# Optimization experiments

Measured on AMD Instinct MI355X. Metric: run time of the kernel, lower is better.

## Reference

```python
import jax, jax.numpy as jnp
import numpy as np

N, T, F_IN = 20000, 13, 3
E = 320000
NB, NL = 4, 2
C_RES, C_DIL, C_SKIP, C_END = 32, 32, 256, 512
KSZ, KHOP = 2, 4
N_PRED, N_OUT = 12, 2
L = NB * NL
DILS = [2 ** i for _ in range(NB) for i in range(NL)]  # [1,2,1,2,1,2,1,2]
EPS = 1e-5


def _dconv(x, w, d):
    # x: [N,C,T], w: [O,I,K]; valid dilated conv -> [N,O,T-(K-1)*d]
    return jax.lax.conv_general_dilated(x, w, (1,), 'VALID', rhs_dilation=(d,),
                                        dimension_numbers=('NCH', 'OIH', 'NCH'))


def _forward(inputs, edge_src, edge_dst, enter_w, enter_b, filt_w, filt_b, gate_w, gate_b,
             gc_w, gc_b, skip_w, skip_b, bn_g, bn_b, out1_w, out1_b, out2_w, out2_b):
    # inputs: [N,T,F] -> x: [N,C_RES,T] via 1x1 conv (enter)
    x = jnp.einsum('of,ntf->not', enter_w, inputs) + enter_b[None, :, None]
    deg = jax.ops.segment_sum(jnp.ones((E,), x.dtype), edge_dst, num_segments=N)
    deg = jnp.maximum(deg, 1.0)[:, None, None]

    def propagate(h):  # [N,t,C]: mean over incoming edges (normalized diffusion step)
        return jax.ops.segment_sum(h[edge_src], edge_dst, num_segments=N) / deg

    skip = jnp.zeros((N, C_SKIP, T), x.dtype)
    for l in range(L):
        d = DILS[l]
        f = jnp.tanh(_dconv(x, filt_w[l], d) + filt_b[l][None, :, None])
        g = jax.nn.sigmoid(_dconv(x, gate_w[l], d) + gate_b[l][None, :, None])
        h = f * g                                   # [N,C_DIL,t]
        t = h.shape[-1]
        skip = skip[..., -t:] + jnp.einsum('oc,nct->not', skip_w[l], h) + skip_b[l][None, :, None]
        # K-hop graph diffusion conv on [N,t,C]
        hh = h.transpose(0, 2, 1)
        acc = jnp.einsum('ntc,co->nto', hh, gc_w[l, 0])
        cur = hh
        for k in range(1, KHOP):
            cur = propagate(cur)
            acc = acc + jnp.einsum('ntc,co->nto', cur, gc_w[l, k])
        acc = acc + gc_b[l]
        x = acc.transpose(0, 2, 1) + x[..., -t:]    # residual add
        # BatchNorm1d over (N, t) per channel (training-mode batch stats)
        mu = x.mean(axis=(0, 2), keepdims=True)
        var = x.var(axis=(0, 2), keepdims=True)
        x = bn_g[l][None, :, None] * (x - mu) * jax.lax.rsqrt(var + EPS) + bn_b[l][None, :, None]
    y = jax.nn.relu(skip)                           # [N,C_SKIP,1]
    y = jax.nn.relu(jnp.einsum('oc,nct->not', out1_w, y) + out1_b[None, :, None])
    y = jnp.einsum('oc,nct->not', out2_w, y) + out2_b[None, :, None]  # [N,n_pred*n_out,1]
    return y.reshape(N, N_PRED, -1)


def setup_inputs() -> dict:
    key = jax.random.key(0)
    ks = jax.random.split(key, 12)
    s = 0.05
    f32 = jnp.float32
    return {
        'inputs': jax.random.normal(ks[0], (N, T, F_IN), f32),
        'edge_src': jax.random.randint(ks[1], (E,), 0, N),
        'edge_dst': jax.random.randint(ks[2], (E,), 0, N),
        'enter_w': jax.random.normal(ks[3], (C_RES, F_IN), f32) * s,
        'enter_b': jnp.zeros((C_RES,), f32),
        'filt_w': jax.random.normal(ks[4], (L, C_DIL, C_RES, KSZ), f32) * s,
        'filt_b': jnp.zeros((L, C_DIL), f32),
        'gate_w': jax.random.normal(ks[5], (L, C_DIL, C_RES, KSZ), f32) * s,
        'gate_b': jnp.zeros((L, C_DIL), f32),
        'gc_w': jax.random.normal(ks[6], (L, KHOP, C_DIL, C_RES), f32) * s,
        'gc_b': jnp.zeros((L, C_RES), f32),
        'skip_w': jax.random.normal(ks[7], (L, C_SKIP, C_DIL), f32) * s,
        'skip_b': jnp.zeros((L, C_SKIP), f32),
        'bn_g': jnp.ones((L, C_RES), f32),
        'bn_b': jnp.zeros((L, C_RES), f32),
        'out1_w': jax.random.normal(ks[8], (C_END, C_SKIP), f32) * s,
        'out1_b': jnp.zeros((C_END,), f32),
        'out2_w': jax.random.normal(ks[9], (N_PRED * N_OUT, C_END), f32) * s,
        'out2_b': jnp.zeros((N_PRED * N_OUT,), f32),
    }


def reference(inputs, edge_src, edge_dst, enter_w, enter_b, filt_w, filt_b, gate_w, gate_b,
              gc_w, gc_b, skip_w, skip_b, bn_g, bn_b, out1_w, out1_b, out2_w, out2_b):
    return _forward(inputs, edge_src, edge_dst, enter_w, enter_b, filt_w, filt_b, gate_w, gate_b,
                    gc_w, gc_b, skip_w, skip_b, bn_g, bn_b, out1_w, out1_b, out2_w, out2_b)
```

## Files before the change

kernel.cpp:

```cpp
#include <hip/hip_runtime.h>
#include <cmath>

constexpr int N = 20000, T = 13, E = 320000;
constexpr int NB_SCAN = (N + 255) / 256;
constexpr int NPART = 64;
typedef unsigned int uint32;

typedef __attribute__((ext_vector_type(8))) short short8;
typedef __attribute__((ext_vector_type(4))) float f32x4;

__device__ __forceinline__ unsigned short f2bf(float f) {
  unsigned int u = __float_as_uint(f);
  unsigned int r = (u + 0x7FFFu + ((u >> 16) & 1u)) >> 16;
  return (unsigned short)r;
}
__device__ __forceinline__ float bflo(uint32 v) { return __uint_as_float(v << 16); }
__device__ __forceinline__ float bfhi(uint32 v) { return __uint_as_float(v & 0xFFFF0000u); }
__device__ __forceinline__ uint32 packbf(float lo, float hi) {
  return (uint32)f2bf(lo) | ((uint32)f2bf(hi) << 16);
}

constexpr size_t WALIGN = 512;
constexpr size_t align_up(size_t x) { return (x + WALIGN - 1) & ~(WALIGN - 1); }

constexpr size_t XA_OFF  = 0;
constexpr size_t X_SZ    = align_up((size_t)N * 13 * 32 * 4);
constexpr size_t XB_OFF  = XA_OFF + X_SZ;
constexpr size_t H_OFF   = XB_OFF + X_SZ;
constexpr size_t H_SZ    = align_up((size_t)N * 12 * 32 * 4);
constexpr size_t C1_OFF  = H_OFF + H_SZ;
constexpr size_t C2_OFF  = C1_OFF + H_SZ;
constexpr size_t C3_OFF  = C2_OFF + H_SZ;
constexpr size_t HL_OFF  = C3_OFF + H_SZ;
constexpr size_t HL_SZ   = align_up((size_t)N * 256 * 4);
constexpr size_t W2P_OFF = HL_OFF + HL_SZ;
constexpr size_t SB_OFF  = W2P_OFF + align_up(8192 * 4);
constexpr size_t SUMS_OFF = SB_OFF + align_up(256 * 4);
constexpr size_t PAR_OFF  = SUMS_OFF + align_up(8 * NPART * 64 * 4);
constexpr size_t CNT_OFF  = PAR_OFF + align_up(9 * 64 * 4);
constexpr size_t ROW_OFF  = CNT_OFF + align_up((size_t)N * 4);
constexpr size_t FILL_OFF = ROW_OFF + align_up((size_t)(N + 1) * 4);
constexpr size_t COL_OFF  = FILL_OFF + align_up((size_t)N * 4);
constexpr size_t DEG_OFF  = COL_OFF + align_up((size_t)E * 4);
constexpr size_t BP_OFF   = DEG_OFF + align_up((size_t)N * 4);
constexpr size_t CP_OFF   = BP_OFF + align_up(8 * 2048 * 4);
constexpr size_t BW1_OFF  = CP_OFF + align_up(8 * 2176 * 4);
constexpr size_t BW2_OFF  = BW1_OFF + align_up(32768 * 4);
constexpr size_t BS_OFF   = BW2_OFF + align_up(65536 * 4);
constexpr size_t S_OFF  = C2_OFF;

constexpr int SU_CNT1 = 20;
constexpr int SU_SUM1 = SU_CNT1 + 32;
constexpr int SU_OUT1 = SU_SUM1 + 469;
constexpr int SU_PAR1 = SU_OUT1 + 1;
constexpr int SU_GCW1 = SU_PAR1 + 64;
constexpr int SU_BW11 = SU_GCW1 + 128;
constexpr int SU_BW21 = SU_BW11 + 256;
constexpr int SU_W21  = SU_BW21 + 32;
constexpr int SU_SB1  = SU_W21 + 1;
constexpr int SU_CV1  = SU_SB1 + 9;
constexpr int SU_EN1  = SU_CV1 + 16250;

__global__ __launch_bounds__(256) void k_setup(
    const float* __restrict__ inputs, const float* __restrict__ enter_w, const float* __restrict__ enter_b,
    const float* __restrict__ filt_w, const float* __restrict__ filt_b,
    const float* __restrict__ gate_w, const float* __restrict__ gate_b,
    const float* __restrict__ gc_w, const float* __restrict__ skip_w, const float* __restrict__ skip_b,
    const float* __restrict__ out1_w, const float* __restrict__ out2_w,
    int* __restrict__ cnt, float* __restrict__ sums,
    float* __restrict__ dout, int out_sz,
    float* __restrict__ par, uint32* __restrict__ bp, uint32* __restrict__ bw1,
    uint32* __restrict__ bw2, uint32* __restrict__ w2p, float* __restrict__ sbias,
    uint32* __restrict__ cpack, uint32* __restrict__ x) {
  int b = blockIdx.x, tid = threadIdx.x;
  if (b < SU_CNT1) {
    int i = b * 256 + tid;
    if (i < 5000) ((int4*)cnt)[i] = make_int4(0, 0, 0, 0);
  } else if (b < SU_SUM1) {
    int i = (b - SU_CNT1) * 256 + tid;
    if (i < 8192) ((float4*)sums)[i] = make_float4(0.f, 0.f, 0.f, 0.f);
  } else if (b < SU_OUT1) {
    int i = (b - SU_SUM1) * 256 + tid;
    if (i < (out_sz >> 2)) ((float4*)dout)[i] = make_float4(0.f, 0.f, 0.f, 0.f);
  } else if (b < SU_PAR1) {
    if (tid < 64) par[tid] = (tid < 32) ? 1.0f : 0.0f;
  } else if (b < SU_GCW1) {
    int idx = (b - SU_PAR1) * 256 + tid;
    int w4 = idx & 3, lane = (idx >> 2) & 63, hh = (idx >> 8) & 1, s = (idx >> 9) & 3, l = idx >> 11;
    int n = lane & 15, q = lane >> 4;
    int k0 = q * 8 + w4 * 2, o = hh * 16 + n;
    const float* g = gc_w + (((size_t)(l * 4 + s) * 32 + k0) * 32 + o);
    bp[idx] = packbf(g[0], g[32]);
  } else if (b < SU_BW11) {
    int idx = (b - SU_GCW1) * 256 + tid;
    int w4 = idx & 3, lane = (idx >> 2) & 63, ks = (idx >> 8) & 7, ot = idx >> 11;
    int n = lane & 15, q = lane >> 4;
    int c = q * 8 + w4 * 2, o = ot * 16 + n;
    const float* wr = skip_w + ((size_t)ks * 256 + o) * 32 + c;
    bw1[idx] = packbf(wr[0], wr[1]);
  } else if (b < SU_BW21) {
    int idx = (b - SU_BW11) * 256 + tid;
    int w4 = idx & 3, lane = (idx >> 2) & 63, ks = (idx >> 8) & 7, ot = idx >> 11;
    int n = lane & 15, q = lane >> 4;
    int k = ks * 32 + q * 8 + w4 * 2;
    const float* wr = out1_w + (size_t)(ot * 16 + n) * 256 + k;
    bw2[idx] = packbf(wr[0], wr[1]);
  } else if (b < SU_W21) {
    int idx = (b - SU_BW21) * 256 + tid;
    int w4 = idx & 3, lane = (idx >> 2) & 63, ks = (idx >> 8) & 15, ot = idx >> 12;
    int n = lane & 15, q = lane >> 4;
    int k = ks * 32 + q * 8 + w4 * 2;
    int o = ot * 16 + n;
    float v0 = 0.0f, v1 = 0.0f;
    if (o < 24) { const float* wr = out2_w + (size_t)o * 512 + k; v0 = wr[0]; v1 = wr[1]; }
    w2p[idx] = packbf(v0, v1);
  } else if (b < SU_SB1) {
    float s = 0.0f;
    for (int l = 0; l < 8; l++) s += skip_b[l * 256 + tid];
    sbias[tid] = s;
  } else if (b < SU_CV1) {
    int i = (b - SU_SB1) * 256 + tid;
    if (i < 2048) {
      int w4 = i & 3, lane = (i >> 2) & 63, hh = (i >> 8) & 1, ktap = (i >> 9) & 1, sel = i >> 10;
      int n = lane & 15, q = lane >> 4;
      int c0 = q * 8 + w4 * 2, o = hh * 16 + n;
      const float* w = sel ? gate_w : filt_w;
      float v0 = w[((size_t)o * 32 + c0) * 2 + ktap];
      float v1 = w[((size_t)o * 32 + c0 + 1) * 2 + ktap];
      cpack[i] = packbf(v0, v1);
    } else if (i < 2112) {
      int j = i - 2048; int sel = j >> 5; int o = j & 31;
      ((float*)cpack)[2048 + j] = sel ? gate_b[o] : filt_b[o];
    }
  } else {
    int idx = (b - SU_CV1) * 256 + tid;
    int cw = idx & 15; int tmp = idx >> 4; int t = tmp % 13; int n = tmp / 13;
    int c0 = cw * 2;
    const float* ip = inputs + (size_t)n * (13 * 3) + t * 3;
    float v0 = enter_b[c0]     + enter_w[c0 * 3 + 0]       * ip[0] + enter_w[c0 * 3 + 1]       * ip[1] + enter_w[c0 * 3 + 2]       * ip[2];
    float v1 = enter_b[c0 + 1] + enter_w[(c0 + 1) * 3 + 0] * ip[0] + enter_w[(c0 + 1) * 3 + 1] * ip[1] + enter_w[(c0 + 1) * 3 + 2] * ip[2];
    x[idx] = packbf(v0, v1);
  }
}

__global__ void k_count(const int* __restrict__ dst, int* __restrict__ cnt) {
  int i = blockIdx.x * 256 + threadIdx.x;
  if (i < E) atomicAdd(&cnt[dst[i]], 1);
}

__global__ __launch_bounds__(256) void k_scan1(const int* __restrict__ cnt, int* __restrict__ bsum) {
  __shared__ int sc[256];
  int t = threadIdx.x; int idx = blockIdx.x * 256 + t;
  int v = (idx < N) ? cnt[idx] : 0;
  sc[t] = v; __syncthreads();
  for (int off = 1; off < 256; off <<= 1) {
    int u = (t >= off) ? sc[t - off] : 0;
    __syncthreads();
    sc[t] += u;
    __syncthreads();
  }
  if (t == 255) bsum[blockIdx.x] = sc[255];
}

__global__ __launch_bounds__(256) void k_scan3(const int* __restrict__ cnt, const int* __restrict__ bsum,
                                               int* __restrict__ rowptr, int* __restrict__ fill,
                                               float* __restrict__ deginv) {
  __shared__ int sc[256];
  __shared__ int bo[128];
  int t = threadIdx.x; int idx = blockIdx.x * 256 + t;
  if (t < 128) bo[t] = (t < NB_SCAN) ? bsum[t] : 0;
  int v = (idx < N) ? cnt[idx] : 0;
  sc[t] = v; __syncthreads();
  for (int off = 1; off < 128; off <<= 1) {
    int u1 = (t < 128 && t >= off) ? bo[t - off] : 0;
    int u2 = (t >= off) ? sc[t - off] : 0;
    __syncthreads();
    if (t < 128) bo[t] += u1;
    sc[t] += u2;
    __syncthreads();
  }
  {
    int u2 = (t >= 128) ? sc[t - 128] : 0;
    __syncthreads();
    sc[t] += u2;
    __syncthreads();
  }
  if (idx < N) {
    int myoff = bo[blockIdx.x] - bsum[blockIdx.x];
    int run = myoff + sc[t] - v;
    rowptr[idx] = run; fill[idx] = run;
    deginv[idx] = 1.0f / (float)(v > 1 ? v : 1);
  }
  if (blockIdx.x == 0 && t == 0) rowptr[N] = bo[NB_SCAN - 1];
}

__global__ void k_scatter(const int* __restrict__ src, const int* __restrict__ dst,
                          int* __restrict__ fill, int* __restrict__ col) {
  int i = blockIdx.x * 256 + threadIdx.x;
  if (i < E) { int d = dst[i]; int p = atomicAdd(&fill[d], 1); col[p] = src[i]; }
}

template <int TIN, int TOUT, int D>
__global__ __launch_bounds__(256, 4) void k_conv(const uint32* __restrict__ x,
    const uint32* __restrict__ cpbuf, int layer,
    uint32* __restrict__ h, uint32* __restrict__ hlast) {
  constexpr int RS = 34;
  __shared__ float xst[128 * RS];
  int tid = threadIdx.x;
  int wave = tid >> 6, lane = tid & 63;
  int m = lane & 15, q = lane >> 4;
  int nrows = N * TOUT;
  int base = blockIdx.x * 128;

  const uint32* cp = cpbuf + (size_t)layer * 2176;
  short8 bf[2][2][2];
#pragma unroll
  for (int sel = 0; sel < 2; sel++)
#pragma unroll
    for (int kt = 0; kt < 2; kt++)
#pragma unroll
      for (int hh = 0; hh < 2; hh++)
        bf[sel][kt][hh] = *(const short8*)(cp + (size_t)(((sel * 2 + kt) * 2 + hh) * 64 + lane) * 4);
  const float* bias = (const float*)(cp + 2048);
  float fb0 = bias[m], fb1 = bias[16 + m], gb0 = bias[32 + m], gb1 = bias[48 + m];

#pragma unroll
  for (int tile = 0; tile < 2; tile++) {
    int row = base + wave * 32 + tile * 16 + m;
    bool valid = row < nrows;
    int rr = valid ? row : 0;
    int n = rr / TOUT, tt = rr - n * TOUT;
    const uint32* xr = x + ((size_t)n * TIN + tt) * 16 + q * 4;
    short8 a0 = {0,0,0,0,0,0,0,0}, aD = {0,0,0,0,0,0,0,0};
    if (valid) { a0 = *(const short8*)xr; aD = *(const short8*)(xr + D * 16); }
    f32x4 aF0 = {0.f,0.f,0.f,0.f}, aF1 = {0.f,0.f,0.f,0.f};
    f32x4 aG0 = {0.f,0.f,0.f,0.f}, aG1 = {0.f,0.f,0.f,0.f};
    aF0 = __builtin_amdgcn_mfma_f32_16x16x32_bf16(a0, bf[0][0][0], aF0, 0, 0, 0);
    aF0 = __builtin_amdgcn_mfma_f32_16x16x32_bf16(aD, bf[0][1][0], aF0, 0, 0, 0);
    aF1 = __builtin_amdgcn_mfma_f32_16x16x32_bf16(a0, bf[0][0][1], aF1, 0, 0, 0);
    aF1 = __builtin_amdgcn_mfma_f32_16x16x32_bf16(aD, bf[0][1][1], aF1, 0, 0, 0);
    aG0 = __builtin_amdgcn_mfma_f32_16x16x32_bf16(a0, bf[1][0][0], aG0, 0, 0, 0);
    aG0 = __builtin_amdgcn_mfma_f32_16x16x32_bf16(aD, bf[1][1][0], aG0, 0, 0, 0);
    aG1 = __builtin_amdgcn_mfma_f32_16x16x32_bf16(a0, bf[1][0][1], aG1, 0, 0, 0);
    aG1 = __builtin_amdgcn_mfma_f32_16x16x32_bf16(aD, bf[1][1][1], aG1, 0, 0, 0);
#pragma unroll
    for (int r = 0; r < 4; r++) {
      int lrow = wave * 32 + tile * 16 + q * 4 + r;
      float F0 = aF0[r] + fb0, G0 = aG0[r] + gb0;
      float F1 = aF1[r] + fb1, G1 = aG1[r] + gb1;
      float af0 = fabsf(F0), ef0 = __expf(-2.0f * af0);
      float th0 = copysignf((1.0f - ef0) / (1.0f + ef0), F0);
      float hv0 = th0 * (1.0f / (1.0f + __expf(-G0)));
      float af1 = fabsf(F1), ef1 = __expf(-2.0f * af1);
      float th1 = copysignf((1.0f - ef1) / (1.0f + ef1), F1);
      float hv1 = th1 * (1.0f / (1.0f + __expf(-G1)));
      xst[lrow * RS + m]      = hv0;
      xst[lrow * RS + 16 + m] = hv1;
    }
  }
  __syncthreads();
  {
    uint2* outp = (uint2*)h;
#pragma unroll
    for (int it = 0; it < 4; it++) {
      int l = it * 256 + tid;
      int g = base * 8 + l;
      if (g < nrows * 8) {
        int rl = l >> 3, j4 = l & 7;
        float2 a = *(const float2*)&xst[rl * RS + j4 * 4];
        float2 b = *(const float2*)&xst[rl * RS + j4 * 4 + 2];
        uint2 pv = make_uint2(packbf(a.x, a.y), packbf(b.x, b.y));
        outp[g] = pv;
        int grow = base + rl;
        int node = grow / TOUT, tt = grow - node * TOUT;
        if (tt == TOUT - 1) {
          *(uint2*)(hlast + (size_t)node * 128 + layer * 16 + j4 * 2) = pv;
        }
      }
    }
  }
}

template <int F>
__global__ __launch_bounds__(256) void k_hop(const uint32* __restrict__ in, uint32* __restrict__ out,
    const int* __restrict__ rowptr, const int* __restrict__ col, const float* __restrict__ deginv) {
  constexpr int F2 = F / 2;
  constexpr int NW = (F2 + 63) / 64;
  int wid = (blockIdx.x * 256 + threadIdx.x) >> 6;
  int lane = threadIdx.x & 63;
  if (wid >= N) return;
  int s = rowptr[wid], e = rowptr[wid + 1];
  float alo[NW], ahi[NW];
#pragma unroll
  for (int k = 0; k < NW; k++) { alo[k] = 0.0f; ahi[k] = 0.0f; }
  int idx = s;
  for (; idx + 7 < e; idx += 8) {
    const uint32* p[8];
#pragma unroll
    for (int q = 0; q < 8; q++) p[q] = in + (size_t)col[idx + q] * F2;
    uint32 v[8][NW];
#pragma unroll
    for (int q = 0; q < 8; q++) {
#pragma unroll
      for (int k = 0; k < NW; k++) {
        int j = k * 64 + lane;
        v[q][k] = (j < F2) ? p[q][j] : 0u;
      }
    }
#pragma unroll
    for (int k = 0; k < NW; k++) {
      alo[k] += ((bflo(v[0][k]) + bflo(v[1][k])) + (bflo(v[2][k]) + bflo(v[3][k]))) +
                ((bflo(v[4][k]) + bflo(v[5][k])) + (bflo(v[6][k]) + bflo(v[7][k])));
      ahi[k] += ((bfhi(v[0][k]) + bfhi(v[1][k])) + (bfhi(v[2][k]) + bfhi(v[3][k]))) +
                ((bfhi(v[4][k]) + bfhi(v[5][k])) + (bfhi(v[6][k]) + bfhi(v[7][k])));
    }
  }
  for (; idx + 3 < e; idx += 4) {
    const uint32* p0 = in + (size_t)col[idx] * F2;
    const uint32* p1 = in + (size_t)col[idx + 1] * F2;
    const uint32* p2 = in + (size_t)col[idx + 2] * F2;
    const uint32* p3 = in + (size_t)col[idx + 3] * F2;
#pragma unroll
    for (int k = 0; k < NW; k++) {
      int j = k * 64 + lane;
      if (j < F2) {
        uint32 v0 = p0[j], v1 = p1[j], v2 = p2[j], v3 = p3[j];
        alo[k] += (bflo(v0) + bflo(v1)) + (bflo(v2) + bflo(v3));
        ahi[k] += (bfhi(v0) + bfhi(v1)) + (bfhi(v2) + bfhi(v3));
      }
    }
  }
  for (; idx < e; ++idx) {
    const uint32* p = in + (size_t)col[idx] * F2;
#pragma unroll
    for (int k = 0; k < NW; k++) {
      int j = k * 64 + lane;
      if (j < F2) { uint32 v = p[j]; alo[k] += bflo(v); ahi[k] += bfhi(v); }
    }
  }
  float inv = deginv[wid];
  uint32* q = out + (size_t)wid * F2;
#pragma unroll
  for (int k = 0; k < NW; k++) {
    int j = k * 64 + lane;
    if (j < F2) q[j] = packbf(alo[k] * inv, ahi[k] * inv);
  }
}

template <int TIN, int TOUT>
__global__ __launch_bounds__(256, 4) void k_combine(const uint32* __restrict__ h,
    const uint32* __restrict__ c1, const uint32* __restrict__ c2, const uint32* __restrict__ c3,
    const uint32* __restrict__ bpack, const float* __restrict__ gcb,
    const uint32* __restrict__ xcur, int layer,
    const float* __restrict__ par,
    uint32* __restrict__ xnext, float* __restrict__ sums) {
  constexpr int RS = 34;
  __shared__ float xst[128 * RS];
  __shared__ float pbuf[96];
  __shared__ float r1s[32], r2s[32];
  int tid = threadIdx.x;
  if (tid < 32) {
    pbuf[tid]      = gcb[layer * 32 + tid];
    pbuf[32 + tid] = par[layer * 64 + tid];
    pbuf[64 + tid] = par[layer * 64 + 32 + tid];
    r1s[tid] = 0.0f; r2s[tid] = 0.0f;
  }

  int nrows = N * TOUT;
  int base = blockIdx.x * 128;
  int wave = tid >> 6, lane = tid & 63;
  int m = lane & 15, q = lane >> 4;

  const uint32* bp = bpack + (size_t)layer * 2048;
  short8 bf[4][2];
#pragma unroll
  for (int s = 0; s < 4; s++)
#pragma unroll
    for (int hh = 0; hh < 2; hh++)
      bf[s][hh] = *(const short8*)(bp + (size_t)((s * 2 + hh) * 64 + lane) * 4);

  f32x4 acc[2][2] = {{{0.f,0.f,0.f,0.f},{0.f,0.f,0.f,0.f}},{{0.f,0.f,0.f,0.f},{0.f,0.f,0.f,0.f}}};
  const uint32* srcs[4] = { h, c1, c2, c3 };
#pragma unroll
  for (int s = 0; s < 4; s++) {
    const uint32* sp = srcs[s];
#pragma unroll
    for (int t = 0; t < 2; t++) {
      int row = base + wave * 32 + t * 16 + m;
      short8 af = {0,0,0,0,0,0,0,0};
      if (row < nrows) af = *(const short8*)(sp + (size_t)row * 16 + q * 4);
      acc[t][0] = __builtin_amdgcn_mfma_f32_16x16x32_bf16(af, bf[s][0], acc[t][0], 0, 0, 0);
      acc[t][1] = __builtin_amdgcn_mfma_f32_16x16x32_bf16(af, bf[s][1], acc[t][1], 0, 0, 0);
    }
  }

  __syncthreads();
#pragma unroll
  for (int t = 0; t < 2; t++)
#pragma unroll
    for (int hh = 0; hh < 2; hh++)
#pragma unroll
      for (int r = 0; r < 4; r++)
        xst[(wave * 32 + t * 16 + q * 4 + r) * RS + hh * 16 + m] = acc[t][hh][r];
  __syncthreads();

  constexpr int toff = TIN - TOUT;
  int rg = tid >> 3, oq = tid & 7;
  float gb0 = pbuf[oq * 4 + 0], gb1 = pbuf[oq * 4 + 1], gb2 = pbuf[oq * 4 + 2], gb3 = pbuf[oq * 4 + 3];
  float sc0 = pbuf[32 + oq * 4 + 0], sc1 = pbuf[32 + oq * 4 + 1], sc2 = pbuf[32 + oq * 4 + 2], sc3 = pbuf[32 + oq * 4 + 3];
  float sh0 = pbuf[64 + oq * 4 + 0], sh1 = pbuf[64 + oq * 4 + 1], sh2 = pbuf[64 + oq * 4 + 2], sh3 = pbuf[64 + oq * 4 + 3];
  float s1[4] = {0.f, 0.f, 0.f, 0.f}, s2[4] = {0.f, 0.f, 0.f, 0.f};
#pragma unroll
  for (int i = 0; i < 4; i++) {
    int r = rg + 32 * i;
    int row = base + r;
    bool act = row < nrows;
    float2 aa = *(const float2*)&xst[r * RS + oq * 4];
    float2 ab = *(const float2*)&xst[r * RS + oq * 4 + 2];
    float xr0 = 0.f, xr1 = 0.f, xr2 = 0.f, xr3 = 0.f;
    if (act) {
      int node = row / TOUT, t_ = row - node * TOUT;
      const uint32* rp = xcur + ((size_t)node * TIN + toff + t_) * 16 + oq * 2;
      uint32 va = rp[0], vb = rp[1];
      xr0 = bflo(va); xr1 = bfhi(va); xr2 = bflo(vb); xr3 = bfhi(vb);
    }
    float v0 = aa.x + gb0 + sc0 * xr0 + sh0;
    float v1 = aa.y + gb1 + sc1 * xr1 + sh1;
    float v2 = ab.x + gb2 + sc2 * xr2 + sh2;
    float v3 = ab.y + gb3 + sc3 * xr3 + sh3;
    *(float2*)&xst[r * RS + oq * 4]     = make_float2(v0, v1);
    *(float2*)&xst[r * RS + oq * 4 + 2] = make_float2(v2, v3);
    if (act) {
      s1[0] += v0; s1[1] += v1; s1[2] += v2; s1[3] += v3;
      s2[0] += v0 * v0; s2[1] += v1 * v1; s2[2] += v2 * v2; s2[3] += v3 * v3;
    }
  }
#pragma unroll
  for (int j = 0; j < 4; j++) {
    atomicAdd(&r1s[oq * 4 + j], s1[j]);
    atomicAdd(&r2s[oq * 4 + j], s2[j]);
  }
  __syncthreads();

  {
    uint2* outp = (uint2*)xnext;
#pragma unroll
    for (int it = 0; it < 4; it++) {
      int l = it * 256 + tid;
      int g = base * 8 + l;
      if (g < nrows * 8) {
        int rl = l >> 3, j4 = l & 7;
        float2 a = *(const float2*)&xst[rl * RS + j4 * 4];
        float2 b = *(const float2*)&xst[rl * RS + j4 * 4 + 2];
        outp[g] = make_uint2(packbf(a.x, a.y), packbf(b.x, b.y));
      }
    }
  }
  {
    int part = blockIdx.x & (NPART - 1);
    float* sp = sums + ((size_t)layer * NPART + part) * 64;
    if (tid < 32) atomicAdd(&sp[tid], r1s[tid]);
    else if (tid < 64) atomicAdd(&sp[tid], r2s[tid - 32]);
  }
}

__global__ __launch_bounds__(256) void k_bnprep(const float* __restrict__ sums,
    const float* __restrict__ bng, const float* __restrict__ bnb, float* __restrict__ par,
    const float* __restrict__ fw, const float* __restrict__ fb,
    const float* __restrict__ gw, const float* __restrict__ gb,
    uint32* __restrict__ cpack, int layer, int tout) {
  __shared__ float red1[8][32];
  __shared__ float red2[8][32];
  __shared__ float pb[64];
  int tid = threadIdx.x;
  {
    int o = tid & 31, grp = tid >> 5;
    float t1 = 0.f, t2 = 0.f;
    const float* lp = sums + (size_t)layer * NPART * 64;
    for (int p = grp; p < NPART; p += 8) {
      t1 += lp[p * 64 + o];
      t2 += lp[p * 64 + 32 + o];
    }
    red1[grp][o] = t1; red2[grp][o] = t2;
  }
  __syncthreads();
  if (tid < 32) {
    float t1 = 0.f, t2 = 0.f;
#pragma unroll
    for (int g = 0; g < 8; g++) { t1 += red1[g][tid]; t2 += red2[g][tid]; }
    float cnt = (float)N * (float)tout;
    float mu = t1 / cnt;
    float var = t2 / cnt - mu * mu;
    float sc = bng[layer * 32 + tid] * rsqrtf(var + 1e-5f);
    float sh = bnb[layer * 32 + tid] - mu * sc;
    par[(layer + 1) * 64 + tid] = sc;
    par[(layer + 1) * 64 + 32 + tid] = sh;
    pb[tid] = sc; pb[32 + tid] = sh;
  }
  __syncthreads();
  int nl = layer + 1;
  uint32* cbase = cpack + (size_t)nl * 2176;
  for (int tix = tid; tix < 2048 + 64; tix += 256) {
    if (tix < 2048) {
      int w4 = tix & 3, lane2 = (tix >> 2) & 63, hh2 = (tix >> 8) & 1, ktap = (tix >> 9) & 1, sel = tix >> 10;
      int n2 = lane2 & 15, q2 = lane2 >> 4;
      int c0 = q2 * 8 + w4 * 2, o = hh2 * 16 + n2;
      const float* w = sel ? gw : fw;
      float v0 = w[(((size_t)nl * 32 + o) * 32 + c0) * 2 + ktap] * pb[c0];
      float v1 = w[(((size_t)nl * 32 + o) * 32 + c0 + 1) * 2 + ktap] * pb[c0 + 1];
      cbase[tix] = packbf(v0, v1);
    } else {
      int i = tix - 2048; int sel = i >> 5; int o = i & 31;
      const float* w = sel ? gw : fw;
      const float* b = sel ? gb : fb;
      float s = b[nl * 32 + o];
      for (int c = 0; c < 32; c++) {
        float sh2 = pb[32 + c];
        s += (w[(((size_t)nl * 32 + o) * 32 + c) * 2 + 0] +
              w[(((size_t)nl * 32 + o) * 32 + c) * 2 + 1]) * sh2;
      }
      ((float*)cbase)[2048 + i] = s;
    }
  }
}

__global__ __launch_bounds__(256) void k_gemm1(const uint32* __restrict__ A,
    const uint32* __restrict__ bp, const float* __restrict__ bias, uint32* __restrict__ Sb) {
  constexpr int RS = 68;
  __shared__ float xst[128 * RS];
  int tid = threadIdx.x;
  int wave = tid >> 6, lane = tid & 63;
  int m = lane & 15, q = lane >> 4;
  int base = blockIdx.x * 128;
  int ot0 = blockIdx.y * 8;

  f32x4 acc[2][8];
#pragma unroll
  for (int t = 0; t < 2; t++)
#pragma unroll
    for (int nt = 0; nt < 8; nt++) acc[t][nt] = (f32x4){0.f, 0.f, 0.f, 0.f};

  int row0 = base + wave * 32 + m;
  int row1 = row0 + 16;
#pragma unroll 1
  for (int ks = 0; ks < 8; ks++) {
    short8 a0 = {0,0,0,0,0,0,0,0}, a1 = {0,0,0,0,0,0,0,0};
    if (row0 < N) a0 = *(const short8*)(A + (size_t)row0 * 128 + ks * 16 + q * 4);
    if (row1 < N) a1 = *(const short8*)(A + (size_t)row1 * 128 + ks * 16 + q * 4);
#pragma unroll
    for (int nt = 0; nt < 8; nt++) {
      short8 b = *(const short8*)(bp + (size_t)(((ot0 + nt) * 8 + ks) * 64 + lane) * 4);
      acc[0][nt] = __builtin_amdgcn_mfma_f32_16x16x32_bf16(a0, b, acc[0][nt], 0, 0, 0);
      acc[1][nt] = __builtin_amdgcn_mfma_f32_16x16x32_bf16(a1, b, acc[1][nt], 0, 0, 0);
    }
  }

#pragma unroll
  for (int half = 0; half < 2; half++) {
    if (half) __syncthreads();
#pragma unroll
    for (int t = 0; t < 2; t++)
#pragma unroll
      for (int nn = 0; nn < 4; nn++) {
        float bv = bias[blockIdx.y * 128 + (half * 4 + nn) * 16 + m];
#pragma unroll
        for (int r = 0; r < 4; r++) {
          float v = acc[t][half * 4 + nn][r] + bv;
          xst[(wave * 32 + t * 16 + q * 4 + r) * RS + nn * 16 + m] = fmaxf(v, 0.0f);
        }
      }
    __syncthreads();
#pragma unroll
    for (int it = 0; it < 8; it++) {
      int l = it * 256 + tid;
      int rl = l >> 4, c4 = l & 15;
      int grow = base + rl;
      if (grow < N) {
        float2 a = *(const float2*)&xst[rl * RS + c4 * 4];
        float2 b = *(const float2*)&xst[rl * RS + c4 * 4 + 2];
        *(uint2*)(Sb + (size_t)grow * 128 + blockIdx.y * 64 + half * 32 + c4 * 2) =
            make_uint2(packbf(a.x, a.y), packbf(b.x, b.y));
      }
    }
  }
}

__global__ __launch_bounds__(256) void k_gemm2f(const uint32* __restrict__ A,
    const uint32* __restrict__ bp, const float* __restrict__ bias,
    const uint32* __restrict__ w2p, const float* __restrict__ b2, float* __restrict__ out) {
  constexpr int RS = 68;
  __shared__ float xst[128 * RS];
  int tid = threadIdx.x;
  int wave = tid >> 6, lane = tid & 63;
  int m = lane & 15, q = lane >> 4;
  int base = blockIdx.x * 128;
  int ot0 = blockIdx.y * 8;

  f32x4 acc[2][8];
#pragma unroll
  for (int t = 0; t < 2; t++)
#pragma unroll
    for (int nt = 0; nt < 8; nt++) acc[t][nt] = (f32x4){0.f, 0.f, 0.f, 0.f};

  int row0 = base + wave * 32 + m;
  int row1 = row0 + 16;
#pragma unroll 1
  for (int ks = 0; ks < 8; ks++) {
    short8 a0 = {0,0,0,0,0,0,0,0}, a1 = {0,0,0,0,0,0,0,0};
    if (row0 < N) a0 = *(const short8*)(A + (size_t)row0 * 128 + ks * 16 + q * 4);
    if (row1 < N) a1 = *(const short8*)(A + (size_t)row1 * 128 + ks * 16 + q * 4);
#pragma unroll
    for (int nt = 0; nt < 8; nt++) {
      short8 b = *(const short8*)(bp + (size_t)(((ot0 + nt) * 8 + ks) * 64 + lane) * 4);
      acc[0][nt] = __builtin_amdgcn_mfma_f32_16x16x32_bf16(a0, b, acc[0][nt], 0, 0, 0);
      acc[1][nt] = __builtin_amdgcn_mfma_f32_16x16x32_bf16(a1, b, acc[1][nt], 0, 0, 0);
    }
  }

  f32x4 acc2[2][2];
#pragma unroll
  for (int t = 0; t < 2; t++)
#pragma unroll
    for (int o2 = 0; o2 < 2; o2++) acc2[t][o2] = (f32x4){0.f, 0.f, 0.f, 0.f};

#pragma unroll
  for (int half = 0; half < 2; half++) {
    if (half) __syncthreads();
#pragma unroll
    for (int t = 0; t < 2; t++)
#pragma unroll
      for (int nn = 0; nn < 4; nn++) {
        float bv = bias[blockIdx.y * 128 + (half * 4 + nn) * 16 + m];
#pragma unroll
        for (int r = 0; r < 4; r++) {
          float v = acc[t][half * 4 + nn][r] + bv;
          xst[(wave * 32 + t * 16 + q * 4 + r) * RS + nn * 16 + m] = fmaxf(v, 0.0f);
        }
      }
    __syncthreads();
#pragma unroll
    for (int kl = 0; kl < 2; kl++) {
      short8 a2[2];
#pragma unroll
      for (int t = 0; t < 2; t++) {
        const float* xp = &xst[(size_t)(wave * 32 + t * 16 + m) * RS + kl * 32 + q * 8];
        float4 f0 = *(const float4*)xp;
        float4 f1 = *(const float4*)(xp + 4);
        uint32 u[4];
        u[0] = packbf(f0.x, f0.y); u[1] = packbf(f0.z, f0.w);
        u[2] = packbf(f1.x, f1.y); u[3] = packbf(f1.z, f1.w);
        a2[t] = *(const short8*)u;
      }
      int ksg = blockIdx.y * 4 + half * 2 + kl;
#pragma unroll
      for (int o2 = 0; o2 < 2; o2++) {
        short8 b = *(const short8*)(w2p + (size_t)(((o2 * 16 + ksg) * 64 + lane) * 4));
        acc2[0][o2] = __builtin_amdgcn_mfma_f32_16x16x32_bf16(a2[0], b, acc2[0][o2], 0, 0, 0);
        acc2[1][o2] = __builtin_amdgcn_mfma_f32_16x16x32_bf16(a2[1], b, acc2[1][o2], 0, 0, 0);
      }
    }
  }

#pragma unroll
  for (int t = 0; t < 2; t++)
#pragma unroll
    for (int o2 = 0; o2 < 2; o2++) {
      int oc = o2 * 16 + m;
      if (oc < 24) {
#pragma unroll
        for (int r = 0; r < 4; r++) {
          int row = base + wave * 32 + t * 16 + q * 4 + r;
          if (row < N) {
            float v = acc2[t][o2][r];
            if (blockIdx.y == 0) v += b2[oc];
            atomicAdd(&out[(size_t)row * 24 + oc], v);
          }
        }
      }
    }
}

struct Ptrs {
  const float *fw, *fb, *gw, *gb, *gcb, *bng, *bnb;
  const uint32 *bpack;
  uint32 *cpack;
  void *H, *C1, *C2, *C3;
  uint32 *HL;
  float *par, *sums;
  const int *row, *col;
  const float *deg;
};

template <int TIN, int TOUT, int D>
static void run_layer(int layer, bool last, const Ptrs& P, uint32*& xc, uint32*& xn, hipStream_t stream) {
  int cblocks = (N * TOUT + 127) / 128;
  k_conv<TIN, TOUT, D><<<cblocks, 256, 0, stream>>>(xc, P.cpack, layer, (uint32*)P.H, P.HL);
  if (!last) {
    constexpr int F = TOUT * 32;
    int hb = (N * 64 + 255) / 256;
    k_hop<F><<<hb, 256, 0, stream>>>((const uint32*)P.H, (uint32*)P.C1, P.row, P.col, P.deg);
    k_hop<F><<<hb, 256, 0, stream>>>((const uint32*)P.C1, (uint32*)P.C2, P.row, P.col, P.deg);
    k_hop<F><<<hb, 256, 0, stream>>>((const uint32*)P.C2, (uint32*)P.C3, P.row, P.col, P.deg);
    k_combine<TIN, TOUT><<<cblocks, 256, 0, stream>>>((const uint32*)P.H, (const uint32*)P.C1,
                                                      (const uint32*)P.C2, (const uint32*)P.C3,
                                                      P.bpack, P.gcb, xc, layer, P.par, xn, P.sums);
    k_bnprep<<<1, 256, 0, stream>>>(P.sums, P.bng, P.bnb, P.par, P.fw, P.fb, P.gw, P.gb,
                                    P.cpack, layer, TOUT);
    uint32* tmp = xc; xc = xn; xn = tmp;
  }
}

extern "C" void kernel_launch(void* const* d_in, const int* in_sizes, int n_in,
                              void* d_out, int out_size, void* d_ws, size_t ws_size,
                              hipStream_t stream) {
  const float* inputs  = (const float*)d_in[0];
  const int*   esrc    = (const int*)d_in[1];
  const int*   edst    = (const int*)d_in[2];
  const float* enter_w = (const float*)d_in[3];
  const float* enter_b = (const float*)d_in[4];
  const float* filt_w  = (const float*)d_in[5];
  const float* filt_b  = (const float*)d_in[6];
  const float* gate_w  = (const float*)d_in[7];
  const float* gate_b  = (const float*)d_in[8];
  const float* gc_w    = (const float*)d_in[9];
  const float* gc_b    = (const float*)d_in[10];
  const float* skip_w  = (const float*)d_in[11];
  const float* skip_b  = (const float*)d_in[12];
  const float* bn_g    = (const float*)d_in[13];
  const float* bn_b    = (const float*)d_in[14];
  const float* out1_w  = (const float*)d_in[15];
  const float* out1_b  = (const float*)d_in[16];
  const float* out2_w  = (const float*)d_in[17];
  const float* out2_b  = (const float*)d_in[18];

  char* ws = (char*)d_ws;
  uint32* XA = (uint32*)(ws + XA_OFF);
  uint32* XB = (uint32*)(ws + XB_OFF);
  void* H    = (void*)(ws + H_OFF);
  void* C1   = (void*)(ws + C1_OFF);
  void* C2   = (void*)(ws + C2_OFF);
  void* C3   = (void*)(ws + C3_OFF);
  uint32* HLB = (uint32*)(ws + HL_OFF);
  uint32* W2P = (uint32*)(ws + W2P_OFF);
  float* SB  = (float*)(ws + SB_OFF);
  float* SUMS = (float*)(ws + SUMS_OFF);
  float* PAR  = (float*)(ws + PAR_OFF);
  int* CNT  = (int*)(ws + CNT_OFF);
  int* ROW  = (int*)(ws + ROW_OFF);
  int* FILL = (int*)(ws + FILL_OFF);
  int* COL  = (int*)(ws + COL_OFF);
  float* DEG = (float*)(ws + DEG_OFF);
  uint32* BP = (uint32*)(ws + BP_OFF);
  uint32* CP = (uint32*)(ws + CP_OFF);
  uint32* BW1 = (uint32*)(ws + BW1_OFF);
  uint32* BW2 = (uint32*)(ws + BW2_OFF);
  int* BS = (int*)(ws + BS_OFF);
  uint32* Sb  = (uint32*)(ws + S_OFF);

  k_setup<<<SU_EN1, 256, 0, stream>>>(inputs, enter_w, enter_b, filt_w, filt_b, gate_w, gate_b,
                                      gc_w, skip_w, skip_b, out1_w, out2_w,
                                      CNT, SUMS, (float*)d_out, out_size,
                                      PAR, BP, BW1, BW2, W2P, SB, CP, XA);

  k_count<<<(E + 255) / 256, 256, 0, stream>>>(edst, CNT);
  k_scan1<<<NB_SCAN, 256, 0, stream>>>(CNT, BS);
  k_scan3<<<NB_SCAN, 256, 0, stream>>>(CNT, BS, ROW, FILL, DEG);
  k_scatter<<<(E + 255) / 256, 256, 0, stream>>>(esrc, edst, FILL, COL);

  Ptrs P;
  P.fw = filt_w; P.fb = filt_b; P.gw = gate_w; P.gb = gate_b;
  P.gcb = gc_b; P.bng = bn_g; P.bnb = bn_b; P.bpack = BP; P.cpack = CP;
  P.H = H; P.C1 = C1; P.C2 = C2; P.C3 = C3; P.HL = HLB; P.par = PAR; P.sums = SUMS;
  P.row = ROW; P.col = COL; P.deg = DEG;

  uint32* xc = XA; uint32* xn = XB;
  run_layer<13, 12, 1>(0, false, P, xc, xn, stream);
  run_layer<12, 10, 2>(1, false, P, xc, xn, stream);
  run_layer<10, 9, 1>(2, false, P, xc, xn, stream);
  run_layer<9, 7, 2>(3, false, P, xc, xn, stream);
  run_layer<7, 6, 1>(4, false, P, xc, xn, stream);
  run_layer<6, 4, 2>(5, false, P, xc, xn, stream);
  run_layer<4, 3, 1>(6, false, P, xc, xn, stream);
  run_layer<3, 1, 2>(7, true, P, xc, xn, stream);

  dim3 g1((N + 127) / 128, 2);
  k_gemm1<<<g1, 256, 0, stream>>>(HLB, BW1, SB, Sb);
  dim3 g2((N + 127) / 128, 4);
  k_gemm2f<<<g2, 256, 0, stream>>>(Sb, BW2, out1_b, W2P, out2_b, (float*)d_out);
}
```

Baseline: 962.3 us.

## Switch activations to time-major layout and remap hop gather per timestep per XCD

Activations are reordered from node-major [N,T,C] to time-major [T,N,C] across the enter, conv, hop and combine kernels, so row indices map directly without div/mod by TOUT. The hop kernel now assigns each block one timestep slice, spreading timesteps over the eight XCDs via the block index so each XCD's L2 caches a single timestep's feature table. A wave handles one node, and 16 lane groups each gather a 64-byte chunk from different neighbors before a shuffle reduction. The cost is more blocks, with some returning early when the timestep count is not a multiple of eight, plus the need for every consumer to agree on the new layout.

```diff
diff --git a/kernel.cpp b/kernel.cpp
--- a/kernel.cpp
+++ b/kernel.cpp
@@ -134,7 +134,7 @@
     }
   } else {
     int idx = (b - SU_CV1) * 256 + tid;
-    int cw = idx & 15; int tmp = idx >> 4; int t = tmp % 13; int n = tmp / 13;
+    int cw = idx & 15; int tmp = idx >> 4; int t = tmp / N; int n = tmp - t * N;
     int c0 = cw * 2;
     const float* ip = inputs + (size_t)n * (13 * 3) + t * 3;
     float v0 = enter_b[c0]     + enter_w[c0 * 3 + 0]       * ip[0] + enter_w[c0 * 3 + 1]       * ip[1] + enter_w[c0 * 3 + 2]       * ip[2];
@@ -229,10 +229,9 @@
     int row = base + wave * 32 + tile * 16 + m;
     bool valid = row < nrows;
     int rr = valid ? row : 0;
-    int n = rr / TOUT, tt = rr - n * TOUT;
-    const uint32* xr = x + ((size_t)n * TIN + tt) * 16 + q * 4;
+    const uint32* xr = x + (size_t)rr * 16 + q * 4;
     short8 a0 = {0,0,0,0,0,0,0,0}, aD = {0,0,0,0,0,0,0,0};
-    if (valid) { a0 = *(const short8*)xr; aD = *(const short8*)(xr + D * 16); }
+    if (valid) { a0 = *(const short8*)xr; aD = *(const short8*)(xr + (size_t)D * N * 16); }
     f32x4 aF0 = {0.f,0.f,0.f,0.f}, aF1 = {0.f,0.f,0.f,0.f};
     f32x4 aG0 = {0.f,0.f,0.f,0.f}, aG1 = {0.f,0.f,0.f,0.f};
     aF0 = __builtin_amdgcn_mfma_f32_16x16x32_bf16(a0, bf[0][0][0], aF0, 0, 0, 0);
@@ -260,6 +259,7 @@
   }
   __syncthreads();
   {
+    constexpr int HB = (TOUT - 1) * N;
     uint2* outp = (uint2*)h;
 #pragma unroll
     for (int it = 0; it < 4; it++) {
@@ -272,8 +272,8 @@
         uint2 pv = make_uint2(packbf(a.x, a.y), packbf(b.x, b.y));
         outp[g] = pv;
         int grow = base + rl;
-        int node = grow / TOUT, tt = grow - node * TOUT;
-        if (tt == TOUT - 1) {
+        if (grow >= HB) {
+          int node = grow - HB;
           *(uint2*)(hlast + (size_t)node * 128 + layer * 16 + j4 * 2) = pv;
         }
       }
@@ -281,69 +281,44 @@
   }
 }
 
-template <int F>
+template <int TOUT>
 __global__ __launch_bounds__(256) void k_hop(const uint32* __restrict__ in, uint32* __restrict__ out,
     const int* __restrict__ rowptr, const int* __restrict__ col, const float* __restrict__ deginv) {
-  constexpr int F2 = F / 2;
-  constexpr int NW = (F2 + 63) / 64;
-  int wid = (blockIdx.x * 256 + threadIdx.x) >> 6;
-  int lane = threadIdx.x & 63;
-  if (wid >= N) return;
-  int s = rowptr[wid], e = rowptr[wid + 1];
-  float alo[NW], ahi[NW];
-#pragma unroll
-  for (int k = 0; k < NW; k++) { alo[k] = 0.0f; ahi[k] = 0.0f; }
-  int idx = s;
-  for (; idx + 7 < e; idx += 8) {
-    const uint32* p[8];
-#pragma unroll
-    for (int q = 0; q < 8; q++) p[q] = in + (size_t)col[idx + q] * F2;
-    uint32 v[8][NW];
-#pragma unroll
-    for (int q = 0; q < 8; q++) {
-#pragma unroll
-      for (int k = 0; k < NW; k++) {
-        int j = k * 64 + lane;
-        v[q][k] = (j < F2) ? p[q][j] : 0u;
-      }
-    }
-#pragma unroll
-    for (int k = 0; k < NW; k++) {
-      alo[k] += ((bflo(v[0][k]) + bflo(v[1][k])) + (bflo(v[2][k]) + bflo(v[3][k]))) +
-                ((bflo(v[4][k]) + bflo(v[5][k])) + (bflo(v[6][k]) + bflo(v[7][k])));
-      ahi[k] += ((bfhi(v[0][k]) + bfhi(v[1][k])) + (bfhi(v[2][k]) + bfhi(v[3][k]))) +
-                ((bfhi(v[4][k]) + bfhi(v[5][k])) + (bfhi(v[6][k]) + bfhi(v[7][k])));
-    }
-  }
-  for (; idx + 3 < e; idx += 4) {
-    const uint32* p0 = in + (size_t)col[idx] * F2;
-    const uint32* p1 = in + (size_t)col[idx + 1] * F2;
-    const uint32* p2 = in + (size_t)col[idx + 2] * F2;
-    const uint32* p3 = in + (size_t)col[idx + 3] * F2;
-#pragma unroll
-    for (int k = 0; k < NW; k++) {
-      int j = k * 64 + lane;
-      if (j < F2) {
-        uint32 v0 = p0[j], v1 = p1[j], v2 = p2[j], v3 = p3[j];
-        alo[k] += (bflo(v0) + bflo(v1)) + (bflo(v2) + bflo(v3));
-        ahi[k] += (bfhi(v0) + bfhi(v1)) + (bfhi(v2) + bfhi(v3));
-      }
-    }
-  }
-  for (; idx < e; ++idx) {
-    const uint32* p = in + (size_t)col[idx] * F2;
-#pragma unroll
-    for (int k = 0; k < NW; k++) {
-      int j = k * 64 + lane;
-      if (j < F2) { uint32 v = p[j]; alo[k] += bflo(v); ahi[k] += bfhi(v); }
-    }
-  }
-  float inv = deginv[wid];
-  uint32* q = out + (size_t)wid * F2;
-#pragma unroll
-  for (int k = 0; k < NW; k++) {
-    int j = k * 64 + lane;
-    if (j < F2) q[j] = packbf(alo[k] * inv, ahi[k] * inv);
+  constexpr int BPS = N / 4;
+  int b = blockIdx.x;
+  int xcd = b & 7, j = b >> 3;
+  int si = j / BPS;
+  int ts = xcd + 8 * si;
+  if (ts >= TOUT) return;
+  int nb = j - si * BPS;
+  int wave = threadIdx.x >> 6, lane = threadIdx.x & 63;
+  int node = nb * 4 + wave;
+  int g = lane >> 2, c = lane & 3;
+  int s = rowptr[node], e = rowptr[node + 1];
+  const uint4* src = (const uint4*)in + (size_t)ts * N * 4;
+  float l0 = 0.f, h0 = 0.f, l1 = 0.f, h1 = 0.f, l2 = 0.f, h2 = 0.f, l3 = 0.f, h3 = 0.f;
+  for (int idx = s + g; idx < e; idx += 16) {
+    uint4 v = src[(size_t)col[idx] * 4 + c];
+    l0 += bflo(v.x); h0 += bfhi(v.x);
+    l1 += bflo(v.y); h1 += bfhi(v.y);
+    l2 += bflo(v.z); h2 += bfhi(v.z);
+    l3 += bflo(v.w); h3 += bfhi(v.w);
+  }
+#pragma unroll
+  for (int mk = 4; mk <= 32; mk <<= 1) {
+    l0 += __shfl_xor(l0, mk); h0 += __shfl_xor(h0, mk);
+    l1 += __shfl_xor(l1, mk); h1 += __shfl_xor(h1, mk);
+    l2 += __shfl_xor(l2, mk); h2 += __shfl_xor(h2, mk);
+    l3 += __shfl_xor(l3, mk); h3 += __shfl_xor(h3, mk);
+  }
+  if (g == 0) {
+    float inv = deginv[node];
+    uint4 o;
+    o.x = packbf(l0 * inv, h0 * inv);
+    o.y = packbf(l1 * inv, h1 * inv);
+    o.z = packbf(l2 * inv, h2 * inv);
+    o.w = packbf(l3 * inv, h3 * inv);
+    ((uint4*)out)[((size_t)ts * N + node) * 4 + c] = o;
   }
 }
 
@@ -419,8 +394,7 @@
     float2 ab = *(const float2*)&xst[r * RS + oq * 4 + 2];
     float xr0 = 0.f, xr1 = 0.f, xr2 = 0.f, xr3 = 0.f;
     if (act) {
-      int node = row / TOUT, t_ = row - node * TOUT;
-      const uint32* rp = xcur + ((size_t)node * TIN + toff + t_) * 16 + oq * 2;
+      const uint32* rp = xcur + ((size_t)toff * N + row) * 16 + oq * 2;
       uint32 va = rp[0], vb = rp[1];
       xr0 = bflo(va); xr1 = bfhi(va); xr2 = bflo(vb); xr3 = bfhi(vb);
     }
@@ -696,11 +670,10 @@
   int cblocks = (N * TOUT + 127) / 128;
   k_conv<TIN, TOUT, D><<<cblocks, 256, 0, stream>>>(xc, P.cpack, layer, (uint32*)P.H, P.HL);
   if (!last) {
-    constexpr int F = TOUT * 32;
-    int hb = (N * 64 + 255) / 256;
-    k_hop<F><<<hb, 256, 0, stream>>>((const uint32*)P.H, (uint32*)P.C1, P.row, P.col, P.deg);
-    k_hop<F><<<hb, 256, 0, stream>>>((const uint32*)P.C1, (uint32*)P.C2, P.row, P.col, P.deg);
-    k_hop<F><<<hb, 256, 0, stream>>>((const uint32*)P.C2, (uint32*)P.C3, P.row, P.col, P.deg);
+    int hb = 8 * (N / 4) * ((TOUT + 7) / 8);
+    k_hop<TOUT><<<hb, 256, 0, stream>>>((const uint32*)P.H, (uint32*)P.C1, P.row, P.col, P.deg);
+    k_hop<TOUT><<<hb, 256, 0, stream>>>((const uint32*)P.C1, (uint32*)P.C2, P.row, P.col, P.deg);
+    k_hop<TOUT><<<hb, 256, 0, stream>>>((const uint32*)P.C2, (uint32*)P.C3, P.row, P.col, P.deg);
     k_combine<TIN, TOUT><<<cblocks, 256, 0, stream>>>((const uint32*)P.H, (const uint32*)P.C1,
                                                       (const uint32*)P.C2, (const uint32*)P.C3,
                                                       P.bpack, P.gcb, xc, layer, P.par, xn, P.sums);
```

New measurement: 2.072 ms. +115.3%, slower.
